# Kernel tuning notes

Hardware: AMD Instinct MI355X
Metric: run time of the kernel (lower is better)

## Reference

```python
import jax, jax.numpy as jnp
import numpy as np

N_BONDS = 16777216
N_ATOMS = 1048576
N_TYPES = 16


def setup_inputs() -> dict:
    key = jax.random.key(0)
    k1, k2, k3, k4, k5, k6 = jax.random.split(key, 6)
    # bond orders kept strictly positive so BO**p_be2 and its grad are finite
    bo_sigma = jax.random.uniform(k1, (N_BONDS,), jnp.float32, 0.05, 1.0)
    bo_pi = jax.random.uniform(k2, (N_BONDS,), jnp.float32, 0.05, 1.0)
    bo_pipi = jax.random.uniform(k3, (N_BONDS,), jnp.float32, 0.05, 1.0)
    bond_type = jax.random.randint(k4, (N_BONDS,), 0, N_TYPES, jnp.int32)
    atom_i = jax.random.randint(k5, (N_BONDS,), 0, N_ATOMS, jnp.int32)
    # columns: De_sigma, De_pi, De_pipi, p_be1, p_be2 (positive, O(1))
    bond_params = jax.random.uniform(k6, (N_TYPES, 5), jnp.float32, 0.1, 1.0)
    return {
        "bond_type": bond_type,
        "atom_i": atom_i,
        "bo_sigma": bo_sigma,
        "bo_pi": bo_pi,
        "bo_pipi": bo_pipi,
        "bond_params": bond_params,
        "n_atoms": N_ATOMS,
    }


def reference(bond_type, atom_i, bo_sigma, bo_pi, bo_pipi, bond_params, n_atoms):
    # Gather per-bond-type parameters: [E, 5]
    p = bond_params[bond_type]
    de_s, de_p, de_pp, p_be1, p_be2 = (p[:, 0], p[:, 1], p[:, 2], p[:, 3], p[:, 4])
    # ReaxFF bond energy per bond
    e_bond = (-de_s * bo_sigma * jnp.exp(p_be1 * (1.0 - bo_sigma ** p_be2))
              - de_p * bo_pi
              - de_pp * bo_pipi)
    # Scatter-reduce to per-atom energy
    e_atom = jax.ops.segment_sum(e_bond, atom_i, num_segments=n_atoms)
    return e_atom
```

## Files before the change

### kernel.cpp

```cpp
#include <hip/hip_runtime.h>


typedef float f32x4 __attribute__((ext_vector_type(4)));
typedef int   i32x4 __attribute__((ext_vector_type(4)));

#define NB     512
#define RANGE  2048
#define SHIFT  11
#define CB     16384
#define TB     256
#define PADQ   8u

__device__ __forceinline__ float bond_e(int t, float bs, float bp, float bpp,
                                        const float* __restrict__ sp) {
    const float* p = sp + t * 5;
    float de_s = p[0], de_p = p[1], de_pp = p[2], p_be1 = p[3], p_be2 = p[4];
    float pw = __powf(bs, p_be2);
    return -de_s * bs * __expf(p_be1 * (1.0f - pw)) - de_p * bp - de_pp * bpp;
}

__device__ __forceinline__ unsigned f32_to_bf16_bits(float f) {
    unsigned u = __float_as_uint(f);
    return ((u + 0x7FFFu + ((u >> 16) & 1u)) >> 16) & 0xFFFFu;
}

__global__ __launch_bounds__(TB) void count_kernel(
        const i32x4* __restrict__ atom_i, unsigned* __restrict__ counts,
        int round_start) {
    __shared__ unsigned hist[4][NB];
    int tid = threadIdx.x, w = tid >> 6;
    for (int i = tid; i < 4 * NB; i += TB) hist[i >> 9][i & (NB - 1)] = 0u;
    __syncthreads();
    long base4 = ((long)round_start + (long)blockIdx.x * CB) >> 2;
#pragma unroll
    for (int it = 0; it < CB / (TB * 4); ++it) {
        i32x4 a = __builtin_nontemporal_load(&atom_i[base4 + it * TB + tid]);
        atomicAdd(&hist[w][(unsigned)a.x >> SHIFT], 1u);
        atomicAdd(&hist[w][(unsigned)a.y >> SHIFT], 1u);
        atomicAdd(&hist[w][(unsigned)a.z >> SHIFT], 1u);
        atomicAdd(&hist[w][(unsigned)a.w >> SHIFT], 1u);
    }
    __syncthreads();
    for (int b = tid; b < NB; b += TB)
        counts[(size_t)blockIdx.x * NB + b] =
            hist[0][b] + hist[1][b] + hist[2][b] + hist[3][b];
}

__global__ void scan_cols_kernel(const unsigned* __restrict__ counts,
                                 unsigned* __restrict__ offs,
                                 unsigned* __restrict__ total, int nsb) {
    __shared__ unsigned sc[1024];
    int b = blockIdx.x, s = threadIdx.x;
    unsigned v = (counts[(size_t)s * NB + b] + PADQ - 1u) & ~(PADQ - 1u);
    sc[s] = v;
    __syncthreads();
    for (int off = 1; off < nsb; off <<= 1) {
        unsigned t = (s >= off) ? sc[s - off] : 0u;
        __syncthreads();
        sc[s] += t;
        __syncthreads();
    }
    offs[(size_t)s * NB + b] = sc[s] - v;
    if (s == nsb - 1) total[b] = sc[s];
}

__global__ void scan_base_kernel(const unsigned* __restrict__ total,
                                 unsigned* __restrict__ base) {
    __shared__ unsigned sc[NB];
    int b = threadIdx.x;
    unsigned v = total[b];
    sc[b] = v;
    __syncthreads();
    for (int off = 1; off < NB; off <<= 1) {
        unsigned t = (b >= off) ? sc[b - off] : 0u;
        __syncthreads();
        sc[b] += t;
        __syncthreads();
    }
    base[b] = sc[b] - v;
}

__global__ __launch_bounds__(TB) void partition_kernel(
        const i32x4* __restrict__ bt, const i32x4* __restrict__ ai,
        const f32x4* __restrict__ bs_, const f32x4* __restrict__ bp_,
        const f32x4* __restrict__ bpp_, const float* __restrict__ bond_params,
        const unsigned* __restrict__ counts, const unsigned* __restrict__ offs,
        const unsigned* __restrict__ base, unsigned* __restrict__ arena,
        int round_start) {
    __shared__ float    sp[80];
    __shared__ unsigned cnt[NB], lstart[NB], cur[NB], part[TB];
    __shared__ unsigned sorted[CB];

    int tid = threadIdx.x, sb = blockIdx.x;
    if (tid < 80) sp[tid] = bond_params[tid];
    unsigned c0 = counts[(size_t)sb * NB + 2 * tid];
    unsigned c1 = counts[(size_t)sb * NB + 2 * tid + 1];
    cnt[2 * tid] = c0; cnt[2 * tid + 1] = c1;
    part[tid] = c0 + c1;
    __syncthreads();
    for (int off = 1; off < TB; off <<= 1) {
        unsigned t = (tid >= off) ? part[tid - off] : 0u;
        __syncthreads();
        part[tid] += t;
        __syncthreads();
    }
    unsigned excl = part[tid] - (c0 + c1);
    lstart[2 * tid] = excl;          cur[2 * tid] = excl;
    lstart[2 * tid + 1] = excl + c0; cur[2 * tid + 1] = excl + c0;
    __syncthreads();

    long base4 = ((long)round_start + (long)sb * CB) >> 2;
#pragma unroll 2
    for (int it = 0; it < CB / (TB * 4); ++it) {
        long idx = base4 + it * TB + tid;
        i32x4 t  = __builtin_nontemporal_load(&bt[idx]);
        i32x4 a  = __builtin_nontemporal_load(&ai[idx]);
        f32x4 s  = __builtin_nontemporal_load(&bs_[idx]);
        f32x4 p  = __builtin_nontemporal_load(&bp_[idx]);
        f32x4 pp = __builtin_nontemporal_load(&bpp_[idx]);
#pragma unroll
        for (int k = 0; k < 4; ++k) {
            unsigned ak = (unsigned)a[k];
            float e = bond_e(t[k], s[k], p[k], pp[k], sp);
            unsigned b = ak >> SHIFT;
            unsigned pos = atomicAdd(&cur[b], 1u);
            sorted[pos] = ((ak & (RANGE - 1u)) << 16) | f32_to_bf16_bits(e);
        }
    }
    __syncthreads();

    int w = tid >> 6, lane = tid & 63;
    for (int b = w; b < NB; b += 4) {
        unsigned len  = cnt[b];
        unsigned plen = (len + PADQ - 1u) & ~(PADQ - 1u);
        unsigned g    = base[b] + offs[(size_t)sb * NB + b];
        unsigned ls   = lstart[b];
        for (unsigned j = lane; j < plen; j += 64u)
            arena[g + j] = (j < len) ? sorted[ls + j] : 0u;
    }
}

__global__ __launch_bounds__(TB) void accum_kernel(
        const unsigned* __restrict__ arena, const unsigned* __restrict__ base,
        const unsigned* __restrict__ total, float* __restrict__ out,
        int add_prev) {
    __shared__ float acc[4][RANGE];
    int tid = threadIdx.x, w = tid >> 6, b = blockIdx.x;
    for (int i = tid; i < RANGE; i += TB) {
        acc[0][i] = 0.f; acc[1][i] = 0.f; acc[2][i] = 0.f; acc[3][i] = 0.f;
    }
    __syncthreads();
    unsigned s0 = base[b], n = total[b];
    const uint4* src = (const uint4*)(arena + s0);
    for (unsigned j = tid; j < (n >> 2); j += TB) {
        uint4 e = src[j];
        if (e.x) atomicAdd(&acc[w][e.x >> 16], __uint_as_float((e.x & 0xFFFFu) << 16));
        if (e.y) atomicAdd(&acc[w][e.y >> 16], __uint_as_float((e.y & 0xFFFFu) << 16));
        if (e.z) atomicAdd(&acc[w][e.z >> 16], __uint_as_float((e.z & 0xFFFFu) << 16));
        if (e.w) atomicAdd(&acc[w][e.w >> 16], __uint_as_float((e.w & 0xFFFFu) << 16));
    }
    __syncthreads();
    size_t ob = (size_t)b * RANGE;
    for (int i = tid; i < RANGE; i += TB) {
        float v = acc[0][i] + acc[1][i] + acc[2][i] + acc[3][i];
        if (add_prev) v += out[ob + i];
        out[ob + i] = v;
    }
}

__global__ __launch_bounds__(TB) void zero_kernel(f32x4* __restrict__ p, int n4) {
    int i = blockIdx.x * blockDim.x + threadIdx.x;
    if (i < n4) p[i] = (f32x4)(0.f);
}

__global__ __launch_bounds__(TB) void atomic_fallback_kernel(
        const i32x4* __restrict__ bt, const i32x4* __restrict__ ai,
        const f32x4* __restrict__ bs_, const f32x4* __restrict__ bp_,
        const f32x4* __restrict__ bpp_, const float* __restrict__ bond_params,
        float* __restrict__ out, int n4) {
    __shared__ float sp[80];
    if (threadIdx.x < 80) sp[threadIdx.x] = bond_params[threadIdx.x];
    __syncthreads();
    int i = blockIdx.x * blockDim.x + threadIdx.x;
    if (i >= n4) return;
    i32x4 t  = bt[i]; i32x4 a = ai[i];
    f32x4 s  = bs_[i]; f32x4 p = bp_[i]; f32x4 pp = bpp_[i];
    unsafeAtomicAdd(&out[a.x], bond_e(t.x, s.x, p.x, pp.x, sp));
    unsafeAtomicAdd(&out[a.y], bond_e(t.y, s.y, p.y, pp.y, sp));
    unsafeAtomicAdd(&out[a.z], bond_e(t.z, s.z, p.z, pp.z, sp));
    unsafeAtomicAdd(&out[a.w], bond_e(t.w, s.w, p.w, pp.w, sp));
}

extern "C" void kernel_launch(void* const* d_in, const int* in_sizes, int n_in,
                              void* d_out, int out_size, void* d_ws, size_t ws_size,
                              hipStream_t stream) {
    const int*   bond_type   = (const int*)  d_in[0];
    const int*   atom_i      = (const int*)  d_in[1];
    const float* bo_sigma    = (const float*)d_in[2];
    const float* bo_pi       = (const float*)d_in[3];
    const float* bo_pipi     = (const float*)d_in[4];
    const float* bond_params = (const float*)d_in[5];
    float*       e_atom      = (float*)d_out;

    const int n_bonds = in_sizes[0];
    const int n_atoms = out_size;

    int NR = 0;
    if (n_atoms == (NB << SHIFT)) {
        const int cands[4] = {1, 2, 4, 8};
        for (int ci = 0; ci < 4; ++ci) {
            int r = cands[ci];
            if (n_bonds % (r * CB)) continue;
            int cpr = n_bonds / r, nsb = cpr / CB;
            if (nsb > 1024 || nsb < 64) continue;
            size_t arena_worst = (size_t)cpr + (size_t)(PADQ - 1) * NB * nsb;
            size_t need = arena_worst * 4 + 2 * (size_t)nsb * NB * 4 + 2 * (size_t)NB * 4;
            if (need <= ws_size) { NR = r; break; }
        }
    }

    if (NR) {
        const int cpr = n_bonds / NR, nsb = cpr / CB;
        size_t arena_worst = (size_t)cpr + (size_t)(PADQ - 1) * NB * nsb;
        unsigned* arena  = (unsigned*)d_ws;
        unsigned* counts = arena + arena_worst;
        unsigned* offs   = counts + (size_t)nsb * NB;
        unsigned* total  = offs + (size_t)nsb * NB;
        unsigned* basep  = total + NB;
        for (int r = 0; r < NR; ++r) {
            int rs = r * cpr;
            count_kernel<<<nsb, TB, 0, stream>>>((const i32x4*)atom_i, counts, rs);
            scan_cols_kernel<<<NB, nsb, 0, stream>>>(counts, offs, total, nsb);
            scan_base_kernel<<<1, NB, 0, stream>>>(total, basep);
            partition_kernel<<<nsb, TB, 0, stream>>>(
                (const i32x4*)bond_type, (const i32x4*)atom_i,
                (const f32x4*)bo_sigma, (const f32x4*)bo_pi, (const f32x4*)bo_pipi,
                bond_params, counts, offs, basep, arena, rs);
            accum_kernel<<<NB, TB, 0, stream>>>(arena, basep, total, e_atom, r ? 1 : 0);
        }
    } else {
        int zn4 = n_atoms / 4;
        zero_kernel<<<(zn4 + TB - 1) / TB, TB, 0, stream>>>((f32x4*)e_atom, zn4);
        int n4 = n_bonds / 4;
        atomic_fallback_kernel<<<(n4 + TB - 1) / TB, TB, 0, stream>>>(
            (const i32x4*)bond_type, (const i32x4*)atom_i,
            (const f32x4*)bo_sigma, (const f32x4*)bo_pi, (const f32x4*)bo_pipi,
            bond_params, e_atom, n4);
    }
}
```

Before: 491.7 us.

## Halve partition chunk, fuse base scan into consumers, and split flush across quarter-waves

Halves the per-block chunk size so the partition kernel uses less shared memory and launches twice as many blocks, with launch bounds requesting higher occupancy. The separate single-block base scan kernel is removed: partition recomputes the bucket base prefix itself, and accum reduces totals to find its start. The column scan now uses 256 threads, each handling several rows. Bond parameters are packed as float4 in shared memory, and the arena flush assigns 16 lanes per bucket so short buckets waste fewer lanes. In exchange, the redundant scans add work to every block, and the smaller chunks raise the padding overhead and the size of the counts array.

```diff
diff --git a/kernel.cpp b/kernel.cpp
--- a/kernel.cpp
+++ b/kernel.cpp
@@ -3,42 +3,35 @@
 
 typedef float f32x4 __attribute__((ext_vector_type(4)));
 typedef int   i32x4 __attribute__((ext_vector_type(4)));
+typedef unsigned u32;
 
 #define NB     512
 #define RANGE  2048
 #define SHIFT  11
-#define CB     16384
+#define CB     8192
 #define TB     256
 #define PADQ   8u
 
-__device__ __forceinline__ float bond_e(int t, float bs, float bp, float bpp,
-                                        const float* __restrict__ sp) {
-    const float* p = sp + t * 5;
-    float de_s = p[0], de_p = p[1], de_pp = p[2], p_be1 = p[3], p_be2 = p[4];
-    float pw = __powf(bs, p_be2);
-    return -de_s * bs * __expf(p_be1 * (1.0f - pw)) - de_p * bp - de_pp * bpp;
-}
-
-__device__ __forceinline__ unsigned f32_to_bf16_bits(float f) {
-    unsigned u = __float_as_uint(f);
+__device__ __forceinline__ u32 f32_to_bf16_bits(float f) {
+    u32 u = __float_as_uint(f);
     return ((u + 0x7FFFu + ((u >> 16) & 1u)) >> 16) & 0xFFFFu;
 }
 
 __global__ __launch_bounds__(TB) void count_kernel(
-        const i32x4* __restrict__ atom_i, unsigned* __restrict__ counts,
+        const i32x4* __restrict__ atom_i, u32* __restrict__ counts,
         int round_start) {
-    __shared__ unsigned hist[4][NB];
+    __shared__ u32 hist[4][NB];
     int tid = threadIdx.x, w = tid >> 6;
-    for (int i = tid; i < 4 * NB; i += TB) hist[i >> 9][i & (NB - 1)] = 0u;
+    for (int i = tid; i < 4 * NB; i += TB) ((u32*)hist)[i] = 0u;
     __syncthreads();
     long base4 = ((long)round_start + (long)blockIdx.x * CB) >> 2;
 #pragma unroll
     for (int it = 0; it < CB / (TB * 4); ++it) {
         i32x4 a = __builtin_nontemporal_load(&atom_i[base4 + it * TB + tid]);
-        atomicAdd(&hist[w][(unsigned)a.x >> SHIFT], 1u);
-        atomicAdd(&hist[w][(unsigned)a.y >> SHIFT], 1u);
-        atomicAdd(&hist[w][(unsigned)a.z >> SHIFT], 1u);
-        atomicAdd(&hist[w][(unsigned)a.w >> SHIFT], 1u);
+        atomicAdd(&hist[w][(u32)a.x >> SHIFT], 1u);
+        atomicAdd(&hist[w][(u32)a.y >> SHIFT], 1u);
+        atomicAdd(&hist[w][(u32)a.z >> SHIFT], 1u);
+        atomicAdd(&hist[w][(u32)a.w >> SHIFT], 1u);
     }
     __syncthreads();
     for (int b = tid; b < NB; b += TB)
@@ -46,71 +39,82 @@
             hist[0][b] + hist[1][b] + hist[2][b] + hist[3][b];
 }
 
-__global__ void scan_cols_kernel(const unsigned* __restrict__ counts,
-                                 unsigned* __restrict__ offs,
-                                 unsigned* __restrict__ total, int nsb) {
-    __shared__ unsigned sc[1024];
-    int b = blockIdx.x, s = threadIdx.x;
-    unsigned v = (counts[(size_t)s * NB + b] + PADQ - 1u) & ~(PADQ - 1u);
-    sc[s] = v;
-    __syncthreads();
-    for (int off = 1; off < nsb; off <<= 1) {
-        unsigned t = (s >= off) ? sc[s - off] : 0u;
-        __syncthreads();
-        sc[s] += t;
-        __syncthreads();
-    }
-    offs[(size_t)s * NB + b] = sc[s] - v;
-    if (s == nsb - 1) total[b] = sc[s];
-}
-
-__global__ void scan_base_kernel(const unsigned* __restrict__ total,
-                                 unsigned* __restrict__ base) {
-    __shared__ unsigned sc[NB];
-    int b = threadIdx.x;
-    unsigned v = total[b];
-    sc[b] = v;
-    __syncthreads();
-    for (int off = 1; off < NB; off <<= 1) {
-        unsigned t = (b >= off) ? sc[b - off] : 0u;
-        __syncthreads();
-        sc[b] += t;
-        __syncthreads();
-    }
-    base[b] = sc[b] - v;
-}
-
-__global__ __launch_bounds__(TB) void partition_kernel(
+__global__ __launch_bounds__(TB) void scan_cols_kernel(
+        const u32* __restrict__ counts, u32* __restrict__ offs,
+        u32* __restrict__ total, int nsb) {
+    __shared__ u32 sc[TB];
+    int b = blockIdx.x, t = threadIdx.x;
+    int vpt = nsb >> 8;
+    u32 v[16];
+    u32 s = 0;
+    for (int k = 0; k < vpt; ++k) {
+        u32 c = counts[(size_t)(t * vpt + k) * NB + b];
+        c = (c + PADQ - 1u) & ~(PADQ - 1u);
+        v[k] = s; s += c;
+    }
+    sc[t] = s;
+    __syncthreads();
+    for (int off = 1; off < TB; off <<= 1) {
+        u32 u = (t >= off) ? sc[t - off] : 0u;
+        __syncthreads();
+        sc[t] += u;
+        __syncthreads();
+    }
+    u32 excl = sc[t] - s;
+    for (int k = 0; k < vpt; ++k)
+        offs[(size_t)(t * vpt + k) * NB + b] = excl + v[k];
+    if (t == TB - 1) total[b] = sc[t];
+}
+
+__global__ __launch_bounds__(TB, 4) void partition_kernel(
         const i32x4* __restrict__ bt, const i32x4* __restrict__ ai,
         const f32x4* __restrict__ bs_, const f32x4* __restrict__ bp_,
         const f32x4* __restrict__ bpp_, const float* __restrict__ bond_params,
-        const unsigned* __restrict__ counts, const unsigned* __restrict__ offs,
-        const unsigned* __restrict__ base, unsigned* __restrict__ arena,
+        const u32* __restrict__ counts, const u32* __restrict__ offs,
+        const u32* __restrict__ total, u32* __restrict__ arena,
         int round_start) {
-    __shared__ float    sp[80];
-    __shared__ unsigned cnt[NB], lstart[NB], cur[NB], part[TB];
-    __shared__ unsigned sorted[CB];
+    __shared__ u32   sorted[CB];
+    __shared__ u32   cnt[NB], cur[NB], gstart[NB];
+    __shared__ u32   scanb[TB];
+    __shared__ float4 sp_a[16];
+    __shared__ float  sp_b[16];
 
     int tid = threadIdx.x, sb = blockIdx.x;
-    if (tid < 80) sp[tid] = bond_params[tid];
-    unsigned c0 = counts[(size_t)sb * NB + 2 * tid];
-    unsigned c1 = counts[(size_t)sb * NB + 2 * tid + 1];
+    if (tid < 16) {
+        const float* p = bond_params + tid * 5;
+        sp_a[tid] = make_float4(p[0], p[1], p[2], p[3]);
+        sp_b[tid] = p[4];
+    }
+    u32 c0 = counts[(size_t)sb * NB + 2 * tid];
+    u32 c1 = counts[(size_t)sb * NB + 2 * tid + 1];
     cnt[2 * tid] = c0; cnt[2 * tid + 1] = c1;
-    part[tid] = c0 + c1;
+    scanb[tid] = c0 + c1;
     __syncthreads();
     for (int off = 1; off < TB; off <<= 1) {
-        unsigned t = (tid >= off) ? part[tid - off] : 0u;
-        __syncthreads();
-        part[tid] += t;
-        __syncthreads();
-    }
-    unsigned excl = part[tid] - (c0 + c1);
-    lstart[2 * tid] = excl;          cur[2 * tid] = excl;
-    lstart[2 * tid + 1] = excl + c0; cur[2 * tid + 1] = excl + c0;
+        u32 u = (tid >= off) ? scanb[tid - off] : 0u;
+        __syncthreads();
+        scanb[tid] += u;
+        __syncthreads();
+    }
+    u32 excl = scanb[tid] - (c0 + c1);
+    cur[2 * tid] = excl; cur[2 * tid + 1] = excl + c0;
+    __syncthreads();
+    u32 t0 = total[2 * tid], t1 = total[2 * tid + 1];
+    scanb[tid] = t0 + t1;
+    __syncthreads();
+    for (int off = 1; off < TB; off <<= 1) {
+        u32 u = (tid >= off) ? scanb[tid - off] : 0u;
+        __syncthreads();
+        scanb[tid] += u;
+        __syncthreads();
+    }
+    u32 excl2 = scanb[tid] - (t0 + t1);
+    gstart[2 * tid]     = excl2 + offs[(size_t)sb * NB + 2 * tid];
+    gstart[2 * tid + 1] = excl2 + t0 + offs[(size_t)sb * NB + 2 * tid + 1];
     __syncthreads();
 
     long base4 = ((long)round_start + (long)sb * CB) >> 2;
-#pragma unroll 2
+#pragma unroll
     for (int it = 0; it < CB / (TB * 4); ++it) {
         long idx = base4 + it * TB + tid;
         i32x4 t  = __builtin_nontemporal_load(&bt[idx]);
@@ -120,39 +124,51 @@
         f32x4 pp = __builtin_nontemporal_load(&bpp_[idx]);
 #pragma unroll
         for (int k = 0; k < 4; ++k) {
-            unsigned ak = (unsigned)a[k];
-            float e = bond_e(t[k], s[k], p[k], pp[k], sp);
-            unsigned b = ak >> SHIFT;
-            unsigned pos = atomicAdd(&cur[b], 1u);
+            u32 ak = (u32)a[k];
+            float4 pa = sp_a[t[k]];
+            float  pb = sp_b[t[k]];
+            float pw = __powf(s[k], pb);
+            float e  = -pa.x * s[k] * __expf(pa.w * (1.0f - pw))
+                       - pa.y * p[k] - pa.z * pp[k];
+            u32 b = ak >> SHIFT;
+            u32 pos = atomicAdd(&cur[b], 1u);
             sorted[pos] = ((ak & (RANGE - 1u)) << 16) | f32_to_bf16_bits(e);
         }
     }
     __syncthreads();
 
     int w = tid >> 6, lane = tid & 63;
-    for (int b = w; b < NB; b += 4) {
-        unsigned len  = cnt[b];
-        unsigned plen = (len + PADQ - 1u) & ~(PADQ - 1u);
-        unsigned g    = base[b] + offs[(size_t)sb * NB + b];
-        unsigned ls   = lstart[b];
-        for (unsigned j = lane; j < plen; j += 64u)
+    int gi = lane >> 4, j0 = lane & 15;
+    for (int b = w * 4 + gi; b < NB; b += 16) {
+        u32 end = cur[b], len = cnt[b], ls = end - len;
+        u32 plen = (len + PADQ - 1u) & ~(PADQ - 1u);
+        u32 g = gstart[b];
+        for (u32 j = j0; j < plen; j += 16u)
             arena[g + j] = (j < len) ? sorted[ls + j] : 0u;
     }
 }
 
-__global__ __launch_bounds__(TB) void accum_kernel(
-        const unsigned* __restrict__ arena, const unsigned* __restrict__ base,
-        const unsigned* __restrict__ total, float* __restrict__ out,
-        int add_prev) {
+__global__ __launch_bounds__(TB, 4) void accum_kernel(
+        const u32* __restrict__ arena, const u32* __restrict__ total,
+        float* __restrict__ out, int add_prev) {
     __shared__ float acc[4][RANGE];
+    __shared__ u32 red[TB];
     int tid = threadIdx.x, w = tid >> 6, b = blockIdx.x;
+    u32 part = 0;
+    for (int i = tid; i < b; i += TB) part += total[i];
+    red[tid] = part;
     for (int i = tid; i < RANGE; i += TB) {
         acc[0][i] = 0.f; acc[1][i] = 0.f; acc[2][i] = 0.f; acc[3][i] = 0.f;
     }
     __syncthreads();
-    unsigned s0 = base[b], n = total[b];
+    for (int s = TB / 2; s > 0; s >>= 1) {
+        if (tid < s) red[tid] += red[tid + s];
+        __syncthreads();
+    }
+    u32 s0 = red[0];
+    u32 n  = total[b];
     const uint4* src = (const uint4*)(arena + s0);
-    for (unsigned j = tid; j < (n >> 2); j += TB) {
+    for (u32 j = tid; j < (n >> 2); j += TB) {
         uint4 e = src[j];
         if (e.x) atomicAdd(&acc[w][e.x >> 16], __uint_as_float((e.x & 0xFFFFu) << 16));
         if (e.y) atomicAdd(&acc[w][e.y >> 16], __uint_as_float((e.y & 0xFFFFu) << 16));
@@ -185,10 +201,14 @@
     if (i >= n4) return;
     i32x4 t  = bt[i]; i32x4 a = ai[i];
     f32x4 s  = bs_[i]; f32x4 p = bp_[i]; f32x4 pp = bpp_[i];
-    unsafeAtomicAdd(&out[a.x], bond_e(t.x, s.x, p.x, pp.x, sp));
-    unsafeAtomicAdd(&out[a.y], bond_e(t.y, s.y, p.y, pp.y, sp));
-    unsafeAtomicAdd(&out[a.z], bond_e(t.z, s.z, p.z, pp.z, sp));
-    unsafeAtomicAdd(&out[a.w], bond_e(t.w, s.w, p.w, pp.w, sp));
+#pragma unroll
+    for (int k = 0; k < 4; ++k) {
+        const float* pr = sp + t[k] * 5;
+        float pw = __powf(s[k], pr[4]);
+        float e  = -pr[0] * s[k] * __expf(pr[3] * (1.0f - pw))
+                   - pr[1] * p[k] - pr[2] * pp[k];
+        unsafeAtomicAdd(&out[a[k]], e);
+    }
 }
 
 extern "C" void kernel_launch(void* const* d_in, const int* in_sizes, int n_in,
@@ -207,14 +227,14 @@
 
     int NR = 0;
     if (n_atoms == (NB << SHIFT)) {
-        const int cands[4] = {1, 2, 4, 8};
-        for (int ci = 0; ci < 4; ++ci) {
+        const int cands[5] = {1, 2, 4, 8, 16};
+        for (int ci = 0; ci < 5; ++ci) {
             int r = cands[ci];
             if (n_bonds % (r * CB)) continue;
             int cpr = n_bonds / r, nsb = cpr / CB;
-            if (nsb > 1024 || nsb < 64) continue;
+            if (nsb % 256 || nsb < 256 || nsb > 4096) continue;
             size_t arena_worst = (size_t)cpr + (size_t)(PADQ - 1) * NB * nsb;
-            size_t need = arena_worst * 4 + 2 * (size_t)nsb * NB * 4 + 2 * (size_t)NB * 4;
+            size_t need = arena_worst * 4 + 2 * (size_t)nsb * NB * 4 + (size_t)NB * 4;
             if (need <= ws_size) { NR = r; break; }
         }
     }
@@ -222,21 +242,19 @@
     if (NR) {
         const int cpr = n_bonds / NR, nsb = cpr / CB;
         size_t arena_worst = (size_t)cpr + (size_t)(PADQ - 1) * NB * nsb;
-        unsigned* arena  = (unsigned*)d_ws;
-        unsigned* counts = arena + arena_worst;
-        unsigned* offs   = counts + (size_t)nsb * NB;
-        unsigned* total  = offs + (size_t)nsb * NB;
-        unsigned* basep  = total + NB;
+        u32* arena  = (u32*)d_ws;
+        u32* counts = arena + arena_worst;
+        u32* offs   = counts + (size_t)nsb * NB;
+        u32* total  = offs + (size_t)nsb * NB;
         for (int r = 0; r < NR; ++r) {
             int rs = r * cpr;
             count_kernel<<<nsb, TB, 0, stream>>>((const i32x4*)atom_i, counts, rs);
-            scan_cols_kernel<<<NB, nsb, 0, stream>>>(counts, offs, total, nsb);
-            scan_base_kernel<<<1, NB, 0, stream>>>(total, basep);
+            scan_cols_kernel<<<NB, TB, 0, stream>>>(counts, offs, total, nsb);
             partition_kernel<<<nsb, TB, 0, stream>>>(
                 (const i32x4*)bond_type, (const i32x4*)atom_i,
                 (const f32x4*)bo_sigma, (const f32x4*)bo_pi, (const f32x4*)bo_pipi,
-                bond_params, counts, offs, basep, arena, rs);
-            accum_kernel<<<NB, TB, 0, stream>>>(arena, basep, total, e_atom, r ? 1 : 0);
+                bond_params, counts, offs, total, arena, rs);
+            accum_kernel<<<NB, TB, 0, stream>>>(arena, total, e_atom, r ? 1 : 0);
         }
     } else {
         int zn4 = n_atoms / 4;
```

New measurement: 440.0 us. 1.12x faster.
